# Kernel optimization log

Measured on AMD Instinct MI355X. Metric: run time of the kernel, lower is better.

The kernel has to match this reference:

```python
import jax, jax.numpy as jnp
import numpy as np

NBINS = 10
POOL = 8
MAX_ANGLE = float(np.pi)


def _sobel_weight(dtype):
    m = jnp.array([[1.0, 0.0, -1.0], [2.0, 0.0, -2.0], [1.0, 0.0, -1.0]], dtype=dtype)
    # [2, 1, 3, 3]: channel 0 = m, channel 1 = m.T
    return jnp.stack([m, m.T], axis=0)[:, None, :, :]


def setup_inputs() -> dict:
    key = jax.random.key(0)
    x = jax.random.uniform(key, (16, 1, 512, 512), dtype=jnp.float32)
    return {"x": x}


def reference(x):
    w = _sobel_weight(x.dtype)
    # conv2d, stride 1, padding 1 -> gxy: [N, 2, H, W]
    gxy = jax.lax.conv_general_dilated(
        x, w, window_strides=(1, 1), padding=[(1, 1), (1, 1)],
        dimension_numbers=("NCHW", "OIHW", "NCHW"))
    gx = gxy[:, 0]  # [N, H, W]
    gy = gxy[:, 1]
    mag = jnp.sqrt(gx * gx + gy * gy)          # gxy.norm(dim=1)
    phase = jnp.arctan2(gx, gy)
    phase_int = phase / MAX_ANGLE * NBINS      # [N, H, W]
    fl = jnp.mod(jnp.floor(phase_int).astype(jnp.int32), NBINS)
    ce = jnp.mod(jnp.ceil(phase_int).astype(jnp.int32), NBINS)
    # scatter_(set) on zeros then scatter_add_ == sum of two one-hot weighted terms
    oh_f = jax.nn.one_hot(fl, NBINS, dtype=x.dtype, axis=1)  # [N, NBINS, H, W]
    oh_c = jax.nn.one_hot(ce, NBINS, dtype=x.dtype, axis=1)
    out = oh_f * mag[:, None] + oh_c * (1.0 - mag)[:, None]  # [N, NBINS, H, W]
    # AvgPool2d(POOL, stride=POOL)
    n, c, h, wdt = out.shape
    pooled = out.reshape(n, c, h // POOL, POOL, wdt // POOL, POOL).mean(axis=(3, 5))
    return pooled
```

## Files before the change

kernel.cpp:

```cpp
#include <hip/hip_runtime.h>
#include <math.h>

#define THR_BASE 9.42477e-6f
#define KFOLD 256.0f
#define KFOLD_INV 0.00390625f
#define LSTRIDE 532

typedef float v2f __attribute__((ext_vector_type(2)));

__global__ void __launch_bounds__(256) hog_kernel(const float* __restrict__ x,
                                                  float* __restrict__ out) {
    __shared__ float s[10 * LSTRIDE];

    int tid = threadIdx.x;
    int blk = blockIdx.x;
    int ch  = blk & 63;
    int n   = blk >> 6;
    const float* img = x + (size_t)n * (512 * 512);
    int R0 = ch * 8 - 1;

#pragma unroll
    for (int k = 0; k < 5; ++k) {
        int j = tid + k * 256;
        int lrow = j >> 7;
        int cb = j & 127;
        int R = R0 + lrow;
        bool rok = (R >= 0) && (R < 512);
        const float4* gp = (const float4*)(img + (size_t)(rok ? R : 0) * 512) + cb;
        float4 v = *gp;
        float m = rok ? 1.0f : 0.0f;
        int L = lrow * LSTRIDE + 5 + cb * 4;
        s[L + 0] = v.x * m;
        s[L + 1] = v.y * m;
        s[L + 2] = v.z * m;
        s[L + 3] = v.w * m;
    }
    if (tid < 10) {
        s[tid * LSTRIDE + 4]   = 0.0f;
        s[tid * LSTRIDE + 517] = 0.0f;
    }
    __syncthreads();

    int r2   = tid & 3;
    int cw   = tid >> 2;
    int row0 = ch * 8 + r2 * 2;
    int col0 = cw * 8;

    float t0[10], t1[10], t2[10], t3[10];
    {
        int base = (2 * r2) * LSTRIDE + 8 * cw + 4;
#define READROW(DST, D)                                                   \
        {                                                                 \
            const float* rp = &s[base + (D) * LSTRIDE];                   \
            float4 a4 = *(const float4*)(rp);                             \
            float4 b4 = *(const float4*)(rp + 4);                         \
            DST[0] = a4.x; DST[1] = a4.y; DST[2] = a4.z; DST[3] = a4.w;   \
            DST[4] = b4.x; DST[5] = b4.y; DST[6] = b4.z; DST[7] = b4.w;   \
            DST[8] = rp[8]; DST[9] = rp[9];                               \
        }
        READROW(t0, 0)
        READROW(t1, 1)
        READROW(t2, 2)
        READROW(t3, 3)
#undef READROW
    }

    float dd0[10], dd1[10], uu0[10], uu1[10];
#pragma unroll
    for (int c = 0; c < 10; ++c) {
        dd0[c] = fmaf(2.0f, t1[c], t0[c] + t2[c]);
        dd1[c] = fmaf(2.0f, t2[c], t1[c] + t3[c]);
        uu0[c] = t0[c] - t2[c];
        uu1[c] = t1[c] - t3[c];
    }

    float gx[16], gy[16];
#pragma unroll
    for (int c = 0; c < 8; ++c) {
        gx[c]     = dd0[c] - dd0[c + 2];
        gx[8 + c] = dd1[c] - dd1[c + 2];
        gy[c]     = fmaf(2.0f, uu0[c + 1], uu0[c] + uu0[c + 2]);
        gy[8 + c] = fmaf(2.0f, uu1[c + 1], uu1[c] + uu1[c + 2]);
    }

    v2f acc[5];
#pragma unroll
    for (int j = 0; j < 5; ++j) acc[j] = (v2f)(0.0f);
    unsigned bmask = 0u;

#pragma unroll
    for (int p = 0; p < 16; ++p) {
        float gxc = gx[p], gyc = gy[p];
        float mag = __builtin_amdgcn_sqrtf(fmaf(gxc, gxc, gyc * gyc));
        float a = fabsf(gxc), b = fabsf(gyc);

        float m1 = fmaf(a, 0.95105651629515353f, -(b * 0.30901699437494740f));
        float m2 = fmaf(a, 0.80901699437494745f, -(b * 0.58778525229247314f));
        float m3 = fmaf(a, 0.58778525229247314f, -(b * 0.80901699437494745f));
        float m4 = fmaf(a, 0.30901699437494740f, -(b * 0.95105651629515353f));

        int k1 = __float_as_int(m1) >> 31;
        int k2 = __float_as_int(m2) >> 31;
        int k3 = __float_as_int(m3) >> 31;
        int k4 = __float_as_int(m4) >> 31;
        int qm = (__float_as_int(gxc) ^ __float_as_int(gyc)) >> 31;

        int fK = __float_as_int(mag + KFOLD);
        int fA = fK & ~qm;
        int fB = fK & qm;

        v2f v0; v0.x = __int_as_float(fA);      v0.y = __int_as_float(fB);
        v2f v1; v1.x = __int_as_float(fA & ~k1); v1.y = __int_as_float(fB & ~k1);
        v2f v2; v2.x = __int_as_float(fA & ~k2); v2.y = __int_as_float(fB & ~k2);
        v2f v3; v3.x = __int_as_float(fA & ~k3); v3.y = __int_as_float(fB & ~k3);
        v2f v4; v4.x = __int_as_float(fA & ~k4); v4.y = __int_as_float(fB & ~k4);
        acc[0] += v0; acc[1] += v1; acc[2] += v2; acc[3] += v3; acc[4] += v4;

        float dmin = fminf(fminf(fminf(fabsf(m1), fabsf(m2)), fabsf(m3)),
                           fminf(fminf(fabsf(m4), a), b));
        bmask = (dmin < THR_BASE * fmaxf(mag, 1.0f)) ? (bmask | (1u << p)) : bmask;
    }

    while (__any((int)(bmask != 0u))) {
        if (bmask) {
            int p = (int)__builtin_ctz(bmask);
            bmask &= bmask - 1u;
            int prow = row0 + (p >> 3);
            int pc   = col0 + (p & 7);
            int rm = prow - 1, rq = prow + 1;
            int cm = pc - 1, cp = pc + 1;
            bool rmok = rm >= 0, rqok = rq < 512;
            bool cmok = cm >= 0, cpok = cp < 512;
            float w00 = (rmok && cmok) ? img[(size_t)rm * 512 + cm] : 0.0f;
            float w01 = rmok ? img[(size_t)rm * 512 + pc] : 0.0f;
            float w02 = (rmok && cpok) ? img[(size_t)rm * 512 + cp] : 0.0f;
            float w10 = cmok ? img[(size_t)prow * 512 + cm] : 0.0f;
            float w12 = cpok ? img[(size_t)prow * 512 + cp] : 0.0f;
            float w20 = (rqok && cmok) ? img[(size_t)rq * 512 + cm] : 0.0f;
            float w21 = rqok ? img[(size_t)rq * 512 + pc] : 0.0f;
            float w22 = (rqok && cpok) ? img[(size_t)rq * 512 + cp] : 0.0f;

            float gxf = fmaf(2.0f, w10, w00 + w20) - fmaf(2.0f, w12, w02 + w22);
            float gyf = fmaf(2.0f, w01 - w21, (w00 - w20) + (w02 - w22));
            float magf = __builtin_amdgcn_sqrtf(fmaf(gxf, gxf, gyf * gyf));
            int negf = (int)(__float_as_uint(fmaf(fabsf(gxf), 0.95105651629515353f, -(fabsf(gyf) * 0.30901699437494740f))) >> 31)
                     + (int)(__float_as_uint(fmaf(fabsf(gxf), 0.80901699437494745f, -(fabsf(gyf) * 0.58778525229247314f))) >> 31)
                     + (int)(__float_as_uint(fmaf(fabsf(gxf), 0.58778525229247314f, -(fabsf(gyf) * 0.80901699437494745f))) >> 31)
                     + (int)(__float_as_uint(fmaf(fabsf(gxf), 0.30901699437494740f, -(fabsf(gyf) * 0.95105651629515353f))) >> 31);
            bool qqf = (((__float_as_uint(gxf) ^ __float_as_uint(gyf)) >> 31) != 0u);
            int onesf = 4 - negf;

            float uv = -(magf + KFOLD);
#pragma unroll
            for (int j = 0; j < 5; ++j) {
                acc[j].x += (!qqf && j <= onesf) ? uv : 0.0f;
                acc[j].y += ( qqf && j <= onesf) ? uv : 0.0f;
            }

            double gxd = (((((double)w00 - (double)w02) + 2.0 * (double)w10)
                           - 2.0 * (double)w12) + (double)w20) - (double)w22;
            double gyd = (((((double)w00 + 2.0 * (double)w01) + (double)w02)
                           - (double)w20) - 2.0 * (double)w21) - (double)w22;
            bool sideB;
            int onese;
            float mvals;
            if (gxd == 0.0) {
                sideB = false; onese = 0; mvals = 1.0f;
            } else if (gyd == 0.0) {
                sideB = true; onese = 4; mvals = 1.0f;
            } else {
                double ad = fabs(gxd), bd = fabs(gyd);
                double M1 = fma(ad, 0.95105651629515353118, -(bd * 0.30901699437494742410));
                double M2 = fma(ad, 0.80901699437494742410, -(bd * 0.58778525229247312917));
                double M3 = fma(ad, 0.58778525229247312917, -(bd * 0.80901699437494742410));
                double M4 = fma(ad, 0.30901699437494742410, -(bd * 0.95105651629515353118));
                int negd = (int)(M1 < 0.0) + (int)(M2 < 0.0)
                         + (int)(M3 < 0.0) + (int)(M4 < 0.0);
                sideB = (gxd < 0.0) != (gyd < 0.0);
                onese = 4 - negd;
                mvals = magf;
            }
            float av = mvals + KFOLD;
#pragma unroll
            for (int j = 0; j < 5; ++j) {
                acc[j].x += (!sideB && j <= onese) ? av : 0.0f;
                acc[j].y += ( sideB && j <= onese) ? av : 0.0f;
            }
        }
    }

    float Am[5], An[5], Bm[5], Bn[5];
#pragma unroll
    for (int j = 0; j < 5; ++j) {
        float qa = rintf(acc[j].x * KFOLD_INV);
        Am[j] = fmaf(qa, -KFOLD, acc[j].x);
        An[j] = qa;
        float qb = rintf(acc[j].y * KFOLD_INV);
        Bm[j] = fmaf(qb, -KFOLD, acc[j].y);
        Bn[j] = qb;
    }
    float M[10], C[10];
#pragma unroll
    for (int sdx = 0; sdx < 5; ++sdx) {
        float am1 = (sdx < 4) ? Am[sdx + 1] : 0.0f;
        float an1 = (sdx < 4) ? An[sdx + 1] : 0.0f;
        M[sdx] = Am[sdx] - am1;
        C[sdx] = An[sdx] - an1;
        float bm1 = (sdx < 4) ? Bm[sdx + 1] : 0.0f;
        float bn1 = (sdx < 4) ? Bn[sdx + 1] : 0.0f;
        M[9 - sdx] = Bm[sdx] - bm1;
        C[9 - sdx] = Bn[sdx] - bn1;
    }

    float* op = out + (((size_t)n * 10) * 64 + ch) * 64 + cw;
#pragma unroll
    for (int b = 0; b < 10; ++b) {
        int bm1 = (b + 9) % 10;
        float v = (M[b] - M[bm1]) + C[bm1];
        v += __shfl_xor(v, 1);
        v += __shfl_xor(v, 2);
        if (r2 == 0) op[(size_t)b * 4096] = v * (1.0f / 64.0f);
    }
}

extern "C" void kernel_launch(void* const* d_in, const int* in_sizes, int n_in,
                              void* d_out, int out_size, void* d_ws, size_t ws_size,
                              hipStream_t stream) {
    const float* x = (const float*)d_in[0];
    float* out = (float*)d_out;
    const int total = 16 * 64 * 64 * 4;
    hog_kernel<<<total / 256, 256, 0, stream>>>(x, out);
}
```

Measured before the change: 15.23 us.

## Use 512 threads per block, one output row per thread

Doubles the block size to 512 threads so each thread handles one row of 8 pixels instead of two rows of 8. The vertical Sobel reuse across two rows is lost, so shared-memory reads per output pixel rise, but register pressure drops and per-thread latency shortens, with more waves available to hide latency. The pooling reduction gains an extra shuffle stage across 8 lanes, and the tile load loop becomes a non-unrolled strided loop.

```diff
diff --git a/kernel.cpp b/kernel.cpp
--- a/kernel.cpp
+++ b/kernel.cpp
@@ -8,8 +8,8 @@
 
 typedef float v2f __attribute__((ext_vector_type(2)));
 
-__global__ void __launch_bounds__(256) hog_kernel(const float* __restrict__ x,
-                                                  float* __restrict__ out) {
+__global__ void __launch_bounds__(512, 6) hog_kernel(const float* __restrict__ x,
+                                                     float* __restrict__ out) {
     __shared__ float s[10 * LSTRIDE];
 
     int tid = threadIdx.x;
@@ -19,9 +19,7 @@
     const float* img = x + (size_t)n * (512 * 512);
     int R0 = ch * 8 - 1;
 
-#pragma unroll
-    for (int k = 0; k < 5; ++k) {
-        int j = tid + k * 256;
+    for (int j = tid; j < 1280; j += 512) {
         int lrow = j >> 7;
         int cb = j & 127;
         int R = R0 + lrow;
@@ -41,14 +39,14 @@
     }
     __syncthreads();
 
-    int r2   = tid & 3;
-    int cw   = tid >> 2;
-    int row0 = ch * 8 + r2 * 2;
+    int r    = tid & 7;
+    int cw   = tid >> 3;
+    int row  = ch * 8 + r;
     int col0 = cw * 8;
 
-    float t0[10], t1[10], t2[10], t3[10];
+    float t0[10], t1[10], t2[10];
     {
-        int base = (2 * r2) * LSTRIDE + 8 * cw + 4;
+        int base = r * LSTRIDE + 8 * cw + 4;
 #define READROW(DST, D)                                                   \
         {                                                                 \
             const float* rp = &s[base + (D) * LSTRIDE];                   \
@@ -61,26 +59,21 @@
         READROW(t0, 0)
         READROW(t1, 1)
         READROW(t2, 2)
-        READROW(t3, 3)
 #undef READROW
     }
 
-    float dd0[10], dd1[10], uu0[10], uu1[10];
+    float dd[10], uu[10];
 #pragma unroll
     for (int c = 0; c < 10; ++c) {
-        dd0[c] = fmaf(2.0f, t1[c], t0[c] + t2[c]);
-        dd1[c] = fmaf(2.0f, t2[c], t1[c] + t3[c]);
-        uu0[c] = t0[c] - t2[c];
-        uu1[c] = t1[c] - t3[c];
-    }
-
-    float gx[16], gy[16];
+        dd[c] = fmaf(2.0f, t1[c], t0[c] + t2[c]);
+        uu[c] = t0[c] - t2[c];
+    }
+
+    float gx[8], gy[8];
 #pragma unroll
     for (int c = 0; c < 8; ++c) {
-        gx[c]     = dd0[c] - dd0[c + 2];
-        gx[8 + c] = dd1[c] - dd1[c + 2];
-        gy[c]     = fmaf(2.0f, uu0[c + 1], uu0[c] + uu0[c + 2]);
-        gy[8 + c] = fmaf(2.0f, uu1[c + 1], uu1[c] + uu1[c + 2]);
+        gx[c] = dd[c] - dd[c + 2];
+        gy[c] = fmaf(2.0f, uu[c + 1], uu[c] + uu[c + 2]);
     }
 
     v2f acc[5];
@@ -89,7 +82,7 @@
     unsigned bmask = 0u;
 
 #pragma unroll
-    for (int p = 0; p < 16; ++p) {
+    for (int p = 0; p < 8; ++p) {
         float gxc = gx[p], gyc = gy[p];
         float mag = __builtin_amdgcn_sqrtf(fmaf(gxc, gxc, gyc * gyc));
         float a = fabsf(gxc), b = fabsf(gyc);
@@ -125,17 +118,16 @@
         if (bmask) {
             int p = (int)__builtin_ctz(bmask);
             bmask &= bmask - 1u;
-            int prow = row0 + (p >> 3);
-            int pc   = col0 + (p & 7);
-            int rm = prow - 1, rq = prow + 1;
+            int pc = col0 + p;
+            int rm = row - 1, rq = row + 1;
             int cm = pc - 1, cp = pc + 1;
             bool rmok = rm >= 0, rqok = rq < 512;
             bool cmok = cm >= 0, cpok = cp < 512;
             float w00 = (rmok && cmok) ? img[(size_t)rm * 512 + cm] : 0.0f;
             float w01 = rmok ? img[(size_t)rm * 512 + pc] : 0.0f;
             float w02 = (rmok && cpok) ? img[(size_t)rm * 512 + cp] : 0.0f;
-            float w10 = cmok ? img[(size_t)prow * 512 + cm] : 0.0f;
-            float w12 = cpok ? img[(size_t)prow * 512 + cp] : 0.0f;
+            float w10 = cmok ? img[(size_t)row * 512 + cm] : 0.0f;
+            float w12 = cpok ? img[(size_t)row * 512 + cp] : 0.0f;
             float w20 = (rqok && cmok) ? img[(size_t)rq * 512 + cm] : 0.0f;
             float w21 = rqok ? img[(size_t)rq * 512 + pc] : 0.0f;
             float w22 = (rqok && cpok) ? img[(size_t)rq * 512 + cp] : 0.0f;
@@ -219,7 +211,8 @@
         float v = (M[b] - M[bm1]) + C[bm1];
         v += __shfl_xor(v, 1);
         v += __shfl_xor(v, 2);
-        if (r2 == 0) op[(size_t)b * 4096] = v * (1.0f / 64.0f);
+        v += __shfl_xor(v, 4);
+        if (r == 0) op[(size_t)b * 4096] = v * (1.0f / 64.0f);
     }
 }
 
@@ -228,6 +221,5 @@
                               hipStream_t stream) {
     const float* x = (const float*)d_in[0];
     float* out = (float*)d_out;
-    const int total = 16 * 64 * 64 * 4;
-    hog_kernel<<<total / 256, 256, 0, stream>>>(x, out);
+    hog_kernel<<<16 * 64, 512, 0, stream>>>(x, out);
 }
```

After: 16.53 us. 1.09x slower.
